# Kernel optimization log

Measured on AMD Instinct MI355X. Metric: run time of the kernel, lower is better.

The kernel has to match this reference:

```python
import jax, jax.numpy as jnp
import numpy as np

LK = 8  # db4 has 8 taps
LEVEL = 5
# pywt.Wavelet('db4').filter_bank[0] == dec_lo
DB4_LO = np.array([-0.010597401784997278, 0.032883011666982945, 0.030841381835986965,
                   -0.18703481171888114, -0.02798376941698385, 0.6308807679295904,
                   0.7148465705525415, 0.23037781330885523], dtype=np.float32)
DN = ('NCH', 'OIH', 'NCH')


def _wpt_kernels(level):
    # Filter_Free WPT: distinct kernel per child node; parent j even -> (lp, hp), odd -> (hp, lp)
    cmf = (-1.0) ** np.arange(LK)
    k_lp = DB4_LO
    k_hp = (DB4_LO[::-1] * cmf).astype(np.float32)
    ks = []
    for i in range(level):
        rows = []
        for j in range(2 ** i):
            rows += [k_lp, k_hp] if j % 2 == 0 else [k_hp, k_lp]
        ks.append(jnp.asarray(np.stack(rows)))  # [2^(i+1), LK]
    return ks


def setup_inputs() -> dict:
    key = jax.random.key(0)
    kx, kb = jax.random.split(key)
    B, N = 128, 32768
    inp = {'x': jax.random.normal(kx, (B, 1, N), dtype=jnp.float32)}
    for i, K in enumerate(_wpt_kernels(LEVEL)):
        inp[f'k{i + 1}'] = K
    for i in range(LEVEL):
        kb, sub = jax.random.split(kb)
        # small positive thresholds (Act_Init=0 would make the threshold an exact identity)
        inp[f'b{i + 1}'] = 0.1 * jax.random.uniform(sub, (2 ** (i + 1),), dtype=jnp.float32)
    return inp


def _analysis(c, K, b):
    # c: [B, G, M] parents -> [B, 2G, M//2] children; one grouped 8-tap conv for the whole level
    G = c.shape[1]
    cp = jnp.pad(c, ((0, 0), (0, 0), (LK // 2 - 1, LK // 2)))
    y = jax.lax.conv_general_dilated(cp, K[:, None, :], (2,), 'VALID',
                                     feature_group_count=G, dimension_numbers=DN)
    bb = b[None, :, None]
    # symmetric sigmoid soft-threshold (Thresh_SigSym), fused elementwise
    return y * (jax.nn.sigmoid(10.0 * (y - bb)) + jax.nn.sigmoid(-10.0 * (y + bb)))


def _synthesis(y, K):
    # adjoint of the strided analysis conv (conv_transpose): [B, 2G, M] -> [B, G, 2M]
    G = y.shape[1] // 2
    M = y.shape[2]
    W = jnp.flip(K, -1).reshape(G, 2, LK)  # sum the two children of each parent
    out = jax.lax.conv_general_dilated(y, W, (1,), [(LK - 1, LK - 1)], lhs_dilation=(2,),
                                       feature_group_count=G, dimension_numbers=DN)
    pl = LK // 2 - 1  # undo analysis left pad
    return out[:, :, pl:pl + 2 * M]


def reference(x, k1, k2, k3, k4, k5, b1, b2, b3, b4, b5):
    Ks = [k1, k2, k3, k4, k5]
    bs = [b1, b2, b3, b4, b5]
    c = x  # [B, 1, N]
    for K, b in zip(Ks, bs):
        c = _analysis(c, K, b)
    for K in Ks[::-1]:
        c = _synthesis(c, K)
    return c  # [B, 1, N] reconstruction
```

## Files before the change

### kernel.cpp

```cpp
#include <hip/hip_runtime.h>

#define TPB 64

constexpr int NSEQ = 32768;
constexpr int C0   = 1024;
constexpr float SCG = 14.4269504089f;


__device__ __forceinline__ float4 ldf4(const float* p) { return *reinterpret_cast<const float4*>(p); }
__device__ __forceinline__ void   stf4(float* p, const float4 v) { *reinterpret_cast<float4*>(p) = v; }

__device__ __forceinline__ float rfl(float x) {
    return __builtin_bit_cast(float, __builtin_amdgcn_readfirstlane(__builtin_bit_cast(int, x)));
}

__device__ __forceinline__ float gated(float y, float tb) {
    float e1 = __builtin_amdgcn_exp2f(fmaf(y, -SCG, tb));
    float e2 = __builtin_amdgcn_exp2f(fmaf(y,  SCG, tb));
    return y * (__builtin_amdgcn_rcpf(1.f + e1) + __builtin_amdgcn_rcpf(1.f + e2));
}

template<int LEin, int LEout, int P, int PAIRS, int Nlev, bool EDGE, bool LAST>
__device__ __forceinline__ void analysis4(
    const float* __restrict__ in, float* __restrict__ out,
    const float* __restrict__ lp, const float* __restrict__ hp,
    const float* __restrict__ bias, int outBase)
{
    constexpr int TPC = P / 4;
    constexpr int TOT = PAIRS * TPC;
    for (int task = threadIdx.x; task < TOT; task += TPB) {
        const int c  = task / TPC;
        const int i0 = (task - c * TPC) * 4;

        const float* pe = in + c * (2 * LEin) + i0;
        const float* po = pe + LEin;
        float a[8], b[8];
        reinterpret_cast<float4*>(a)[0] = ldf4(pe);
        reinterpret_cast<float4*>(a)[1] = ldf4(pe + 4);
        reinterpret_cast<float4*>(b)[0] = ldf4(po);
        reinterpret_cast<float4*>(b)[1] = ldf4(po + 4);

        const int sw     = c & 1;
        const int ch_lp  = 2 * c + sw;
        const int ch_hp  = 2 * c + 1 - sw;
        const float tb_l = bias[ch_lp];
        const float tb_h = bias[ch_hp];

        float vl[4], vh[4];
#pragma unroll
        for (int r = 0; r < 4; ++r) {
            float yl = 0.f, yh = 0.f;
#pragma unroll
            for (int u = 0; u < 4; ++u) {
                yl = fmaf(a[r + u], lp[2 * u], yl);
                yl = fmaf(b[r + u], lp[2 * u + 1], yl);
                yh = fmaf(a[r + u], hp[2 * u], yh);
                yh = fmaf(b[r + u], hp[2 * u + 1], yh);
            }
            float wl = gated(yl, tb_l);
            float wh = gated(yh, tb_h);
            if (EDGE) {
                const bool ok = ((unsigned)(outBase + i0 + r) < (unsigned)Nlev);
                wl = ok ? wl : 0.f;
                wh = ok ? wh : 0.f;
            }
            vl[r] = wl; vh[r] = wh;
        }

        if (LAST) {
            stf4(out + ch_lp * LEout + i0, make_float4(vl[0], vl[1], vl[2], vl[3]));
            stf4(out + ch_hp * LEout + i0, make_float4(vh[0], vh[1], vh[2], vh[3]));
        } else {
            const int j0 = i0 >> 1;
            float* ol = out + ch_lp * (2 * LEout);
            float* oh = out + ch_hp * (2 * LEout);
            *reinterpret_cast<float2*>(ol + j0)         = make_float2(vl[0], vl[2]);
            *reinterpret_cast<float2*>(ol + LEout + j0) = make_float2(vl[1], vl[3]);
            *reinterpret_cast<float2*>(oh + j0)         = make_float2(vh[0], vh[2]);
            *reinterpret_cast<float2*>(oh + LEout + j0) = make_float2(vh[1], vh[3]);
        }
    }
}

template<int Sin, int Sout, int G, int Nlev, bool EDGE>
__device__ __forceinline__ void synth8(
    const float* __restrict__ in, float* __restrict__ out,
    const float* __restrict__ lp, const float* __restrict__ hp, int outBase)
{
    constexpr int TPG = Sout / 8;
    constexpr int TOT = G * TPG;
    for (int task = threadIdx.x; task < TOT; task += TPB) {
        const int g   = task / TPG;
        const int nl0 = (task - g * TPG) * 8;
        const int sw  = g & 1;

        float ya[8], yb[8];
        {
            const float* p0 = in + (2 * g + sw)     * Sin + nl0 / 2;
            const float* p1 = in + (2 * g + 1 - sw) * Sin + nl0 / 2;
            reinterpret_cast<float4*>(ya)[0] = ldf4(p0);
            reinterpret_cast<float4*>(ya)[1] = ldf4(p0 + 4);
            reinterpret_cast<float4*>(yb)[0] = ldf4(p1);
            reinterpret_cast<float4*>(yb)[1] = ldf4(p1 + 4);
        }

        float o[8];
#pragma unroll
        for (int r = 0; r < 8; ++r) {
            const int jr = (r + 1) >> 1;
            const int kb = 7 - (r & 1);
            float acc = 0.f;
#pragma unroll
            for (int q = 0; q < 4; ++q) {
                acc = fmaf(ya[jr + q], lp[kb - 2 * q], acc);
                acc = fmaf(yb[jr + q], hp[kb - 2 * q], acc);
            }
            if (EDGE) {
                const bool ok = ((unsigned)(outBase + nl0 + r) < (unsigned)Nlev);
                acc = ok ? acc : 0.f;
            }
            o[r] = acc;
        }
        float* op = out + g * Sout + nl0;
        stf4(op,     make_float4(o[0], o[1], o[2], o[3]));
        stf4(op + 4, make_float4(o[4], o[5], o[6], o[7]));
    }
}

template<bool EDGE>
__device__ __forceinline__ void run_chunk(
    const float* __restrict__ xb, float* __restrict__ ob, int s,
    float* __restrict__ bufA, float* __restrict__ bufB,
    const float* __restrict__ lp, const float* __restrict__ hp,
    const float* __restrict__ bss)
{
    const int tid = threadIdx.x;

    {
        const int base = s - 221;
        for (int j = tid; j < 764; j += TPB) {
            const int g0 = base + 2 * j;
            if (EDGE) {
                bufA[j]       = ((unsigned)g0       < (unsigned)NSEQ) ? xb[g0]     : 0.f;
                bufA[764 + j] = ((unsigned)(g0 + 1) < (unsigned)NSEQ) ? xb[g0 + 1] : 0.f;
            } else {
                bufA[j]       = xb[g0];
                bufA[764 + j] = xb[g0 + 1];
            }
        }
    }
    __syncthreads();

    analysis4<764, 380, 760,  1, 16384, EDGE, false>(bufA, bufB, lp, hp, bss + 0,  (s >> 1) - 109);
    __syncthreads();
    analysis4<380, 188, 376,  2,  8192, EDGE, false>(bufB, bufA, lp, hp, bss + 2,  (s >> 2) - 53);
    __syncthreads();
    analysis4<188,  92, 184,  4,  4096, EDGE, false>(bufA, bufB, lp, hp, bss + 6,  (s >> 3) - 25);
    __syncthreads();
    analysis4< 92,  44,  88,  8,  2048, EDGE, false>(bufB, bufA, lp, hp, bss + 14, (s >> 4) - 11);
    __syncthreads();
    analysis4< 44,  40,  40, 16,  1024, EDGE, true >(bufA, bufB, lp, hp, bss + 30, (s >> 5) - 4);
    __syncthreads();

    synth8< 40,  72, 16,  2048, EDGE>(bufB, bufA, lp, hp, (s >> 4) - 4);
    __syncthreads();
    synth8< 72, 136,  8,  4096, EDGE>(bufA, bufB, lp, hp, (s >> 3) - 4);
    __syncthreads();
    synth8<136, 264,  4,  8192, EDGE>(bufB, bufA, lp, hp, (s >> 2) - 4);
    __syncthreads();
    synth8<264, 520,  2, 16384, EDGE>(bufA, bufB, lp, hp, (s >> 1) - 4);
    __syncthreads();

    for (int task = tid; task < 128; task += TPB) {
        const int i0 = task * 8;
        float ya[12], yb[12];
        {
            const float* p0 = bufB + i0 / 2;
            const float* p1 = p0 + 520;
            reinterpret_cast<float4*>(ya)[0] = ldf4(p0);
            reinterpret_cast<float4*>(ya)[1] = ldf4(p0 + 4);
            reinterpret_cast<float4*>(ya)[2] = ldf4(p0 + 8);
            reinterpret_cast<float4*>(yb)[0] = ldf4(p1);
            reinterpret_cast<float4*>(yb)[1] = ldf4(p1 + 4);
            reinterpret_cast<float4*>(yb)[2] = ldf4(p1 + 8);
        }
        float o[8];
#pragma unroll
        for (int r = 0; r < 8; ++r) {
            const int jr = ((r + 1) >> 1) + 2;
            const int kb = 7 - (r & 1);
            float acc = 0.f;
#pragma unroll
            for (int q = 0; q < 4; ++q) {
                acc = fmaf(ya[jr + q], lp[kb - 2 * q], acc);
                acc = fmaf(yb[jr + q], hp[kb - 2 * q], acc);
            }
            o[r] = acc;
        }
        stf4(ob + i0,     make_float4(o[0], o[1], o[2], o[3]));
        stf4(ob + i0 + 4, make_float4(o[4], o[5], o[6], o[7]));
    }
}

__global__ __launch_bounds__(TPB) void wpt_fused(
    const float* __restrict__ x,
    const float* __restrict__ K1, const float* __restrict__ K2,
    const float* __restrict__ K3, const float* __restrict__ K4,
    const float* __restrict__ K5,
    const float* __restrict__ B1, const float* __restrict__ B2,
    const float* __restrict__ B3, const float* __restrict__ B4,
    const float* __restrict__ B5,
    float* __restrict__ out)
{
    __shared__ __align__(16) float bufA[1528];
    __shared__ __align__(16) float bufB[1520];
    __shared__ float bss[62];

    const int tid   = threadIdx.x;
    const int batch = blockIdx.x >> 5;
    const int cid   = blockIdx.x & 31;
    const int s     = cid * C0;

    float lp[8], hp[8];
#pragma unroll
    for (int t = 0; t < 8; ++t) {
        lp[t] = rfl(K1[t]);
        hp[t] = rfl(K1[8 + t]);
    }

    {
        const float* bin[5] = {B1, B2, B3, B4, B5};
        const int boff[5] = {0, 2, 6, 14, 30};
#pragma unroll
        for (int l = 0; l < 5; ++l)
            for (int i = tid; i < (2 << l); i += TPB) bss[boff[l] + i] = SCG * bin[l][i];
    }

    const float* xb = x + batch * NSEQ;
    float* ob = out + batch * NSEQ + s;

    if (cid == 0 || cid == 31)
        run_chunk<true >(xb, ob, s, bufA, bufB, lp, hp, bss);
    else
        run_chunk<false>(xb, ob, s, bufA, bufB, lp, hp, bss);
}

extern "C" void kernel_launch(void* const* d_in, const int* in_sizes, int n_in,
                              void* d_out, int out_size, void* d_ws, size_t ws_size,
                              hipStream_t stream) {
    const int nbatch = in_sizes[0] / NSEQ;
    wpt_fused<<<dim3(nbatch * (NSEQ / C0)), dim3(TPB), 0, stream>>>(
        (const float*)d_in[0],
        (const float*)d_in[1], (const float*)d_in[2],
        (const float*)d_in[3], (const float*)d_in[4],
        (const float*)d_in[5],
        (const float*)d_in[6], (const float*)d_in[7],
        (const float*)d_in[8], (const float*)d_in[9],
        (const float*)d_in[10],
        (float*)d_out);
}
```

Before: 128.1 us.

## Fuse level-5 analysis with first synthesis, widen blocks, vectorize interior loads

Doubles the block size to 128 threads and adds a launch-bounds occupancy hint. Fuses the last analysis level with the first synthesis stage in registers, removing one shared-memory round trip and one barrier. Interior chunks now load input with float4 global reads and deinterleave even/odd samples in registers; only edge chunks keep the bounds-checked scalar path. The cost is higher register pressure and a shuffled shared-buffer ping-pong order that must stay consistent.

```diff
diff --git a/kernel.cpp b/kernel.cpp
--- a/kernel.cpp
+++ b/kernel.cpp
@@ -1,6 +1,6 @@
 #include <hip/hip_runtime.h>
 
-#define TPB 64
+#define TPB 128
 
 constexpr int NSEQ = 32768;
 constexpr int C0   = 1024;
@@ -20,7 +20,7 @@
     return y * (__builtin_amdgcn_rcpf(1.f + e1) + __builtin_amdgcn_rcpf(1.f + e2));
 }
 
-template<int LEin, int LEout, int P, int PAIRS, int Nlev, bool EDGE, bool LAST>
+template<int LEin, int LEout, int P, int PAIRS, int Nlev, bool EDGE>
 __device__ __forceinline__ void analysis4(
     const float* __restrict__ in, float* __restrict__ out,
     const float* __restrict__ lp, const float* __restrict__ hp,
@@ -67,18 +67,82 @@
             vl[r] = wl; vh[r] = wh;
         }
 
-        if (LAST) {
-            stf4(out + ch_lp * LEout + i0, make_float4(vl[0], vl[1], vl[2], vl[3]));
-            stf4(out + ch_hp * LEout + i0, make_float4(vh[0], vh[1], vh[2], vh[3]));
-        } else {
-            const int j0 = i0 >> 1;
-            float* ol = out + ch_lp * (2 * LEout);
-            float* oh = out + ch_hp * (2 * LEout);
-            *reinterpret_cast<float2*>(ol + j0)         = make_float2(vl[0], vl[2]);
-            *reinterpret_cast<float2*>(ol + LEout + j0) = make_float2(vl[1], vl[3]);
-            *reinterpret_cast<float2*>(oh + j0)         = make_float2(vh[0], vh[2]);
-            *reinterpret_cast<float2*>(oh + LEout + j0) = make_float2(vh[1], vh[3]);
-        }
+        const int j0 = i0 >> 1;
+        float* ol = out + ch_lp * (2 * LEout);
+        float* oh = out + ch_hp * (2 * LEout);
+        *reinterpret_cast<float2*>(ol + j0)         = make_float2(vl[0], vl[2]);
+        *reinterpret_cast<float2*>(ol + LEout + j0) = make_float2(vl[1], vl[3]);
+        *reinterpret_cast<float2*>(oh + j0)         = make_float2(vh[0], vh[2]);
+        *reinterpret_cast<float2*>(oh + LEout + j0) = make_float2(vh[1], vh[3]);
+    }
+}
+
+template<bool EDGE>
+__device__ __forceinline__ void fused_l5(
+    const float* __restrict__ in, float* __restrict__ out,
+    const float* __restrict__ lp, const float* __restrict__ hp,
+    const float* __restrict__ bias, int s)
+{
+    for (int task = threadIdx.x; task < 16 * 9; task += TPB) {
+        const int g   = task / 9;
+        const int nl0 = (task - g * 9) * 8;
+        const int j0  = nl0 >> 1;
+
+        const float* pe = in + g * 88 + j0;
+        const float* po = pe + 44;
+        float E[12], O[12];
+        reinterpret_cast<float4*>(E)[0] = ldf4(pe);
+        reinterpret_cast<float4*>(E)[1] = ldf4(pe + 4);
+        reinterpret_cast<float4*>(E)[2] = ldf4(pe + 8);
+        reinterpret_cast<float4*>(O)[0] = ldf4(po);
+        reinterpret_cast<float4*>(O)[1] = ldf4(po + 4);
+        reinterpret_cast<float4*>(O)[2] = ldf4(po + 8);
+
+        const int sw = g & 1;
+        const float tbl = bias[2 * g + sw];
+        const float tbh = bias[2 * g + 1 - sw];
+
+        float ya[8], yb[8];
+#pragma unroll
+        for (int j = 0; j < 8; ++j) {
+            float yl = 0.f, yh = 0.f;
+#pragma unroll
+            for (int u = 0; u < 4; ++u) {
+                yl = fmaf(E[j + u], lp[2 * u], yl);
+                yl = fmaf(O[j + u], lp[2 * u + 1], yl);
+                yh = fmaf(E[j + u], hp[2 * u], yh);
+                yh = fmaf(O[j + u], hp[2 * u + 1], yh);
+            }
+            float wl = gated(yl, tbl);
+            float wh = gated(yh, tbh);
+            if (EDGE) {
+                const bool ok = ((unsigned)((s >> 5) - 4 + j0 + j) < 1024u);
+                wl = ok ? wl : 0.f;
+                wh = ok ? wh : 0.f;
+            }
+            ya[j] = wl; yb[j] = wh;
+        }
+
+        float o[8];
+#pragma unroll
+        for (int r = 0; r < 8; ++r) {
+            const int jr = (r + 1) >> 1;
+            const int kb = 7 - (r & 1);
+            float acc = 0.f;
+#pragma unroll
+            for (int q = 0; q < 4; ++q) {
+                acc = fmaf(ya[jr + q], lp[kb - 2 * q], acc);
+                acc = fmaf(yb[jr + q], hp[kb - 2 * q], acc);
+            }
+            if (EDGE) {
+                const bool ok = ((unsigned)((s >> 4) - 4 + nl0 + r) < 2048u);
+                acc = ok ? acc : 0.f;
+            }
+            o[r] = acc;
+        }
+        float* op = out + g * 72 + nl0;
+        stf4(op,     make_float4(o[0], o[1], o[2], o[3]));
+        stf4(op + 4, make_float4(o[4], o[5], o[6], o[7]));
     }
 }
 
@@ -136,46 +200,50 @@
 {
     const int tid = threadIdx.x;
 
-    {
+    if (EDGE) {
         const int base = s - 221;
         for (int j = tid; j < 764; j += TPB) {
             const int g0 = base + 2 * j;
-            if (EDGE) {
-                bufA[j]       = ((unsigned)g0       < (unsigned)NSEQ) ? xb[g0]     : 0.f;
-                bufA[764 + j] = ((unsigned)(g0 + 1) < (unsigned)NSEQ) ? xb[g0 + 1] : 0.f;
-            } else {
-                bufA[j]       = xb[g0];
-                bufA[764 + j] = xb[g0 + 1];
-            }
-        }
-    }
-    __syncthreads();
-
-    analysis4<764, 380, 760,  1, 16384, EDGE, false>(bufA, bufB, lp, hp, bss + 0,  (s >> 1) - 109);
-    __syncthreads();
-    analysis4<380, 188, 376,  2,  8192, EDGE, false>(bufB, bufA, lp, hp, bss + 2,  (s >> 2) - 53);
-    __syncthreads();
-    analysis4<188,  92, 184,  4,  4096, EDGE, false>(bufA, bufB, lp, hp, bss + 6,  (s >> 3) - 25);
-    __syncthreads();
-    analysis4< 92,  44,  88,  8,  2048, EDGE, false>(bufB, bufA, lp, hp, bss + 14, (s >> 4) - 11);
-    __syncthreads();
-    analysis4< 44,  40,  40, 16,  1024, EDGE, true >(bufA, bufB, lp, hp, bss + 30, (s >> 5) - 4);
-    __syncthreads();
-
-    synth8< 40,  72, 16,  2048, EDGE>(bufB, bufA, lp, hp, (s >> 4) - 4);
-    __syncthreads();
-    synth8< 72, 136,  8,  4096, EDGE>(bufA, bufB, lp, hp, (s >> 3) - 4);
-    __syncthreads();
-    synth8<136, 264,  4,  8192, EDGE>(bufB, bufA, lp, hp, (s >> 2) - 4);
-    __syncthreads();
-    synth8<264, 520,  2, 16384, EDGE>(bufA, bufB, lp, hp, (s >> 1) - 4);
+            bufA[j]       = ((unsigned)g0       < (unsigned)NSEQ) ? xb[g0]     : 0.f;
+            bufA[764 + j] = ((unsigned)(g0 + 1) < (unsigned)NSEQ) ? xb[g0 + 1] : 0.f;
+        }
+    } else {
+        const float* xa = xb + s - 224;
+        for (int t = tid; t < 383; t += TPB) {
+            const float4 v = *reinterpret_cast<const float4*>(xa + 4 * t);
+            if (t > 0) {
+                bufA[2 * t - 1] = v.y;
+                *reinterpret_cast<float2*>(bufA + 764 + 2 * t - 2) = make_float2(v.x, v.z);
+            }
+            if (t < 382) bufA[2 * t] = v.w;
+        }
+    }
+    __syncthreads();
+
+    analysis4<764, 380, 760,  1, 16384, EDGE>(bufA, bufB, lp, hp, bss + 0,  (s >> 1) - 109);
+    __syncthreads();
+    analysis4<380, 188, 376,  2,  8192, EDGE>(bufB, bufA, lp, hp, bss + 2,  (s >> 2) - 53);
+    __syncthreads();
+    analysis4<188,  92, 184,  4,  4096, EDGE>(bufA, bufB, lp, hp, bss + 6,  (s >> 3) - 25);
+    __syncthreads();
+    analysis4< 92,  44,  88,  8,  2048, EDGE>(bufB, bufA, lp, hp, bss + 14, (s >> 4) - 11);
+    __syncthreads();
+
+    fused_l5<EDGE>(bufA, bufB, lp, hp, bss + 30, s);
+    __syncthreads();
+
+    synth8< 72, 136,  8,  4096, EDGE>(bufB, bufA, lp, hp, (s >> 3) - 4);
+    __syncthreads();
+    synth8<136, 264,  4,  8192, EDGE>(bufA, bufB, lp, hp, (s >> 2) - 4);
+    __syncthreads();
+    synth8<264, 520,  2, 16384, EDGE>(bufB, bufA, lp, hp, (s >> 1) - 4);
     __syncthreads();
 
     for (int task = tid; task < 128; task += TPB) {
         const int i0 = task * 8;
         float ya[12], yb[12];
         {
-            const float* p0 = bufB + i0 / 2;
+            const float* p0 = bufA + i0 / 2;
             const float* p1 = p0 + 520;
             reinterpret_cast<float4*>(ya)[0] = ldf4(p0);
             reinterpret_cast<float4*>(ya)[1] = ldf4(p0 + 4);
@@ -202,7 +270,7 @@
     }
 }
 
-__global__ __launch_bounds__(TPB) void wpt_fused(
+__global__ __launch_bounds__(TPB, 6) void wpt_fused(
     const float* __restrict__ x,
     const float* __restrict__ K1, const float* __restrict__ K2,
     const float* __restrict__ K3, const float* __restrict__ K4,
```

After: 124.0 us. 3.2% less time.
